# Kernel optimization log

Measured on AMD Instinct MI355X. Metric: run time of the kernel, lower is better.

The kernel has to match this reference:

```python
import jax, jax.numpy as jnp
import numpy as np

QUANT_DEPTH = 4
EMBED_DIM = 256
N_EMBED = 8192
B, H, W = 8, 32, 32


def setup_inputs() -> dict:
    key = jax.random.key(0)
    k1, k2 = jax.random.split(key)
    x = jax.random.normal(k1, (B, H, W, EMBED_DIM), dtype=jnp.float32)
    codebooks = jax.random.normal(k2, (QUANT_DEPTH, N_EMBED, EMBED_DIM), dtype=jnp.float32)
    return {"x": x, "codebooks": codebooks}


def _nearest_code(flat, cb):
    # flat: [N, D], cb: [K, D] -> idx: [N]
    # ||v - c||^2 = ||v||^2 + ||c||^2 - 2 v.c  (addmm in torch source)
    d = (jnp.sum(flat * flat, axis=1, keepdims=True)
         + jnp.sum(cb * cb, axis=1)[None, :]
         - 2.0 * (flat @ cb.T))  # [N, K]
    return jnp.argmin(d, axis=1)


def reference(x, codebooks):
    Bx, h, w, D = x.shape
    # quantization path is entirely non-differentiable (torch: detach + no_grad)
    resid = jax.lax.stop_gradient(x)
    agg = jnp.zeros_like(resid)
    quant_list = []
    code_list = []
    for i in range(codebooks.shape[0]):
        cb = codebooks[i]                      # [K, D]
        idx = _nearest_code(resid.reshape(-1, D), cb)  # [N]
        quant = cb[idx].reshape(Bx, h, w, D)
        resid = resid - quant
        agg = agg + quant
        quant_list.append(agg)
        code_list.append(idx.reshape(Bx, h, w, 1))
    codes = jnp.concatenate(code_list, axis=-1)  # [B, h, w, depth]
    # commitment loss: mean over depths of mean((x - agg_i.detach())^2)
    commitment_loss = jnp.mean(
        jnp.stack([jnp.mean((x - jax.lax.stop_gradient(q)) ** 2) for q in quant_list]))
    # straight-through estimator
    quants_trunc = x + jax.lax.stop_gradient(quant_list[-1] - x)
    return quants_trunc, commitment_loss, codes
```

## Files before the change

### kernel.cpp

```cpp
#include <hip/hip_runtime.h>

#define DIM   256
#define NVEC  8192
#define NCODE 8192
#define DEPTH 4

#define KBLK  8
#define KC    (NCODE / KBLK)
#define KT    (KC / 128)
#define FCAP  8192
#define FKS   32
#define FV    8
#define KAPPA 0.018f

typedef short  b8 __attribute__((ext_vector_type(8)));
typedef short  b4 __attribute__((ext_vector_type(4)));
typedef float  f4 __attribute__((ext_vector_type(4)));

static __device__ __forceinline__ unsigned short f2bf(float f) {
  unsigned u = __float_as_uint(f);
  return (unsigned short)((u + 0x7FFFu + ((u >> 16) & 1u)) >> 16);
}

static __device__ __forceinline__ void gll16(const void* g, void* l) {
  __builtin_amdgcn_global_load_lds(
      (const __attribute__((address_space(1))) void*)g,
      (__attribute__((address_space(3))) void*)l, 16, 0, 0);
}

__global__ __launch_bounds__(256) void prep_norms(const float* __restrict__ cb_all,
                                                  float* __restrict__ cc,
                                                  float* __restrict__ cchat) {
  int row  = blockIdx.x * 4 + (threadIdx.x >> 6);
  int lane = threadIdx.x & 63;
  float4 v = *(const float4*)&cb_all[(size_t)row * DIM + lane * 4];
  float st = 0.f, sh = 0.f;
  float vv[4] = {v.x, v.y, v.z, v.w};
  #pragma unroll
  for (int j = 0; j < 4; ++j) {
    float hf = __uint_as_float(((unsigned)f2bf(vv[j])) << 16);
    st += vv[j] * vv[j];
    sh += hf * hf;
  }
  #pragma unroll
  for (int off = 32; off > 0; off >>= 1) {
    st += __shfl_down(st, off, 64);
    sh += __shfl_down(sh, off, 64);
  }
  if (lane == 0) { cc[row] = st; cchat[row] = sh; }
}

__global__ __launch_bounds__(256) void prep_depth(const float* __restrict__ cbd,
                                                  unsigned short* __restrict__ cbh,
                                                  float* __restrict__ cbT) {
  __shared__ float ts[64][68];
  const int kb = blockIdx.x >> 2, db = blockIdx.x & 3;
  const int k0 = kb * 64, d0 = db * 64;
  const int t  = threadIdx.x;
  const int r  = t >> 2;
  const int c4 = (t & 3) * 16;

  const float* src = cbd + (size_t)(k0 + r) * DIM + d0 + c4;
  float4 q[4];
  #pragma unroll
  for (int i = 0; i < 4; ++i) q[i] = *(const float4*)(src + i * 4);

  b8 h0, h1;
  #pragma unroll
  for (int j = 0; j < 4; ++j) { h0[j] = (short)f2bf(q[0][j]); h0[4 + j] = (short)f2bf(q[1][j]); }
  #pragma unroll
  for (int j = 0; j < 4; ++j) { h1[j] = (short)f2bf(q[2][j]); h1[4 + j] = (short)f2bf(q[3][j]); }
  *(b8*)&cbh[(size_t)(k0 + r) * DIM + d0 + c4]     = h0;
  *(b8*)&cbh[(size_t)(k0 + r) * DIM + d0 + c4 + 8] = h1;

  #pragma unroll
  for (int i = 0; i < 4; ++i)
    #pragma unroll
    for (int j = 0; j < 4; ++j)
      ts[c4 + i * 4 + j][r] = q[i][j];
  __syncthreads();

  const int dd = t >> 2, kk4 = (t & 3) * 16;
  float* dst = cbT + (size_t)(d0 + dd) * NCODE + k0 + kk4;
  #pragma unroll
  for (int q4 = 0; q4 < 4; ++q4)
    *(float4*)(dst + q4 * 4) = *(const float4*)&ts[dd][kk4 + q4 * 4];
}

__global__ __launch_bounds__(256) void init_kernel(const float* __restrict__ x,
                                                   float* __restrict__ resid,
                                                   unsigned short* __restrict__ rb,
                                                   float* __restrict__ rsum0) {
  int n    = blockIdx.x * 4 + (threadIdx.x >> 6);
  int lane = threadIdx.x & 63;
  float4 v = *(const float4*)&x[(size_t)n * DIM + lane * 4];
  *(float4*)&resid[(size_t)n * DIM + lane * 4] = v;
  b4 hv; hv[0] = (short)f2bf(v.x); hv[1] = (short)f2bf(v.y);
  hv[2] = (short)f2bf(v.z); hv[3] = (short)f2bf(v.w);
  *(b4*)&rb[(size_t)n * DIM + lane * 4] = hv;
  float s = v.x * v.x + v.y * v.y + v.z * v.z + v.w * v.w;
  #pragma unroll
  for (int off = 32; off > 0; off >>= 1) s += __shfl_down(s, off, 64);
  if (lane == 0) rsum0[n] = s;
}

__global__ __launch_bounds__(512, 2) void coarse_kernel(
    const unsigned short* __restrict__ rb,
    const unsigned short* __restrict__ cbh,
    const float* __restrict__ cchat,
    float* __restrict__ pv1, int* __restrict__ pi1, float* __restrict__ pv2,
    int* __restrict__ fcount) {
  __shared__ __align__(16) char lds[65536];

  const int tid  = threadIdx.x;
  const int w    = tid >> 6;
  const int l    = tid & 63;
  const int mw   = w >> 1, kw = w & 1;
  const int mblk = blockIdx.x / KBLK;
  const int kblk = blockIdx.x % KBLK;
  const int m0   = mblk * 128;
  const int K0   = kblk * KC;

  if (blockIdx.x == 0 && tid == 0) *fcount = 0;

  int aoff[2], boff[2], ldst[2];
  #pragma unroll
  for (int it = 0; it < 2; ++it) {
    int o = it * 512 + tid;
    int row = o >> 3, ssl = (o & 7) ^ (row & 7);
    aoff[it] = (m0 + row) * 512 + ssl * 16;
    boff[it] = (K0 + row) * 512 + ssl * 16;
    ldst[it] = o * 16;
  }
  int offA[2][2], offB[4][2];
  #pragma unroll
  for (int mf = 0; mf < 2; ++mf) {
    int row = mw * 32 + mf * 16 + (l & 15);
    int base = row * 128 + (((l >> 4) ^ (row & 7)) * 16);
    offA[mf][0] = base; offA[mf][1] = base ^ 64;
  }
  #pragma unroll
  for (int nf = 0; nf < 4; ++nf) {
    int row = kw * 64 + nf * 16 + (l & 15);
    int base = row * 128 + (((l >> 4) ^ (row & 7)) * 16);
    offB[nf][0] = base; offB[nf][1] = base ^ 64;
  }

  const int kgb = K0 + kw * 64 + (l & 15);

  float tv1[8], tv2[8];
  int   ti1[8];
  #pragma unroll
  for (int s = 0; s < 8; ++s) { tv1[s] = 3.4e38f; tv2[s] = 3.4e38f; ti1[s] = 0; }

  f4 acc[2][4];
  b8 ar[4][2][2];

  #pragma unroll
  for (int it = 0; it < 2; ++it) {
    gll16((const char*)rb  + aoff[it], lds + ldst[it]);
    gll16((const char*)cbh + boff[it], lds + 16384 + ldst[it]);
  }
  __syncthreads();

  for (int kt = 0; kt < KT; ++kt) {
    #pragma unroll
    for (int dt = 0; dt < 4; ++dt) {
      const int buf = dt & 1;
      if (!(kt == KT - 1 && dt == 3)) {
        const int ndt = (dt + 1) & 3;
        const int nb  = ndt & 1;
        const int nktoff = (dt == 3) ? (kt + 1) * 65536 : kt * 65536;
        if (kt == 0 && dt < 3) {
          #pragma unroll
          for (int it = 0; it < 2; ++it)
            gll16((const char*)rb + aoff[it] + ndt * 128,
                  lds + nb * 32768 + ldst[it]);
        }
        #pragma unroll
        for (int it = 0; it < 2; ++it)
          gll16((const char*)cbh + boff[it] + nktoff + ndt * 128,
                lds + nb * 32768 + 16384 + ldst[it]);
      }
      if (dt == 0) {
        #pragma unroll
        for (int i = 0; i < 2; ++i)
          #pragma unroll
          for (int j = 0; j < 4; ++j)
            acc[i][j] = (f4){0.f, 0.f, 0.f, 0.f};
      }
      #pragma unroll
      for (int kk = 0; kk < 2; ++kk) {
        b8 af[2], bb[4];
        if (kt == 0) {
          #pragma unroll
          for (int mf = 0; mf < 2; ++mf) {
            af[mf] = *(const b8*)(lds + buf * 32768 + offA[mf][kk]);
            ar[dt][kk][mf] = af[mf];
          }
        } else {
          #pragma unroll
          for (int mf = 0; mf < 2; ++mf) af[mf] = ar[dt][kk][mf];
        }
        #pragma unroll
        for (int nf = 0; nf < 4; ++nf)
          bb[nf] = *(const b8*)(lds + buf * 32768 + 16384 + offB[nf][kk]);
        #pragma unroll
        for (int mf = 0; mf < 2; ++mf)
          #pragma unroll
          for (int nf = 0; nf < 4; ++nf)
            acc[mf][nf] = __builtin_amdgcn_mfma_f32_16x16x32_bf16(
                af[mf], bb[nf], acc[mf][nf], 0, 0, 0);
      }
      if (dt == 3) {
        float cn[4]; int kg[4];
        #pragma unroll
        for (int nf = 0; nf < 4; ++nf) {
          kg[nf] = kgb + kt * 128 + nf * 16;
          cn[nf] = cchat[kg[nf]];
        }
        #pragma unroll
        for (int mf = 0; mf < 2; ++mf)
          #pragma unroll
          for (int r = 0; r < 4; ++r) {
            const int s0 = mf * 4 + r;
            #pragma unroll
            for (int nf = 0; nf < 4; ++nf) {
              float s = fmaf(-2.f, acc[mf][nf][r], cn[nf]);
              bool  c = s < tv1[s0];
              float m2 = fminf(tv2[s0], s);
              tv2[s0] = c ? tv1[s0] : m2;
              ti1[s0] = c ? kg[nf] : ti1[s0];
              tv1[s0] = c ? s : tv1[s0];
            }
          }
      }
      __syncthreads();
    }
  }

  float* Mv1 = (float*)lds;
  int*   Mi1 = (int*)(lds + 1024);
  float* Mv2 = (float*)(lds + 2048);

  #pragma unroll
  for (int s0 = 0; s0 < 8; ++s0) {
    float v1 = tv1[s0], v2 = tv2[s0];
    int   i1 = ti1[s0];
    #pragma unroll
    for (int m = 1; m < 16; m <<= 1) {
      float qv1 = __shfl_xor(v1, m);
      int   qi1 = __shfl_xor(i1, m);
      float qv2 = __shfl_xor(v2, m);
      bool  qw  = (qv1 < v1) || (qv1 == v1 && qi1 < i1);
      float lose = qw ? v1 : qv1;
      float wv2  = qw ? qv2 : v2;
      v2 = fminf(wv2, lose);
      if (qw) { v1 = qv1; i1 = qi1; }
    }
    if ((l & 15) == 0) {
      int mf = s0 >> 2, r = s0 & 3;
      int rowL = mw * 32 + mf * 16 + (l >> 4) * 4 + r;
      Mv1[rowL * 2 + kw] = v1; Mi1[rowL * 2 + kw] = i1; Mv2[rowL * 2 + kw] = v2;
    }
  }
  __syncthreads();
  if (tid < 128) {
    float a1 = Mv1[tid * 2],     a2 = Mv2[tid * 2];     int a1i = Mi1[tid * 2];
    float b1 = Mv1[tid * 2 + 1], b2 = Mv2[tid * 2 + 1]; int b1i = Mi1[tid * 2 + 1];
    bool  bw = (b1 < a1) || (b1 == a1 && b1i < a1i);
    float v1 = bw ? b1 : a1; int i1 = bw ? b1i : a1i;
    float v2 = fminf(bw ? b2 : a2, bw ? a1 : b1);
    int n = m0 + tid;
    pv1[kblk * NVEC + n] = v1;
    pi1[kblk * NVEC + n] = i1;
    pv2[kblk * NVEC + n] = v2;
  }
}

__global__ __launch_bounds__(256) void merge_kernel(
    const float* __restrict__ pv1, const int* __restrict__ pi1,
    const float* __restrict__ pv2, const float* __restrict__ vnorm,
    int* __restrict__ idx, int* __restrict__ flist, int* __restrict__ fslot,
    int* __restrict__ fcount) {
  int n = blockIdx.x * 256 + threadIdx.x;
  float v1 = 3.4e38f, v2 = 3.4e38f; int i1 = 0;
  #pragma unroll
  for (int kb = 0; kb < KBLK; ++kb) {
    float b1 = pv1[kb * NVEC + n]; int b1i = pi1[kb * NVEC + n];
    float b2 = pv2[kb * NVEC + n];
    bool  bw = (b1 < v1) || (b1 == v1 && b1i < i1);
    float lose = bw ? v1 : b1;
    float wv2  = bw ? b2 : v2;
    v2 = fminf(wv2, lose);
    if (bw) { v1 = b1; i1 = b1i; }
  }
  idx[n] = i1;
  float thr = KAPPA * sqrtf(fmaxf(v1 + vnorm[n], 0.f)) + 1e-5f;
  int slot = -1;
  if (v2 - v1 < thr) {
    slot = atomicAdd(fcount, 1);
    flist[slot] = n;
  }
  fslot[n] = slot;
}

__global__ __launch_bounds__(256, 4) void fb_scan_t(
    const float* __restrict__ cbT, const float* __restrict__ cc,
    const float* __restrict__ resid, const int* __restrict__ flist,
    const int* __restrict__ fcount,
    float* __restrict__ fpv, int* __restrict__ fpi) {
  __shared__ float vsT[DIM][FV + 4];
  __shared__ float mv[FV][4];
  __shared__ int   mi[FV][4];
  const int cnt = min(*fcount, FCAP);
  const int ks = blockIdx.x & (FKS - 1);
  const int t = threadIdx.x;
  const int w = t >> 6, l = t & 63;
  const int k = ks * 256 + t;
  const float cn = cc[k];

  for (int chunk = blockIdx.x >> 5; chunk * FV < cnt; chunk += 256) {
    __syncthreads();
    #pragma unroll
    for (int v = 0; v < FV; ++v) {
      int s = chunk * FV + v;
      int n = flist[s < cnt ? s : chunk * FV];
      vsT[t][v] = resid[(size_t)n * DIM + t];
    }
    __syncthreads();

    float dot[FV];
    #pragma unroll
    for (int v = 0; v < FV; ++v) dot[v] = 0.f;

    #pragma unroll 8
    for (int d = 0; d < DIM; ++d) {
      float cv = cbT[(size_t)d * NCODE + k];
      f4 a0 = *(const f4*)&vsT[d][0];
      f4 a1 = *(const f4*)&vsT[d][4];
      dot[0] = fmaf(cv, a0[0], dot[0]);
      dot[1] = fmaf(cv, a0[1], dot[1]);
      dot[2] = fmaf(cv, a0[2], dot[2]);
      dot[3] = fmaf(cv, a0[3], dot[3]);
      dot[4] = fmaf(cv, a1[0], dot[4]);
      dot[5] = fmaf(cv, a1[1], dot[5]);
      dot[6] = fmaf(cv, a1[2], dot[6]);
      dot[7] = fmaf(cv, a1[3], dot[7]);
    }

    #pragma unroll
    for (int v = 0; v < FV; ++v) {
      float bv = fmaf(-2.f, dot[v], cn);
      int   bi = k;
      #pragma unroll
      for (int m = 1; m < 64; m <<= 1) {
        float qv = __shfl_xor(bv, m);
        int   qi = __shfl_xor(bi, m);
        if (qv < bv || (qv == bv && qi < bi)) { bv = qv; bi = qi; }
      }
      if (l == 0) { mv[v][w] = bv; mi[v][w] = bi; }
    }
    __syncthreads();
    if (t < FV) {
      float bv = mv[t][0]; int bi = mi[t][0];
      #pragma unroll
      for (int ww = 1; ww < 4; ++ww) {
        float qv = mv[t][ww]; int qi = mi[t][ww];
        if (qv < bv || (qv == bv && qi < bi)) { bv = qv; bi = qi; }
      }
      if (chunk * FV + t < cnt) {
        fpv[(size_t)(chunk * FV + t) * FKS + ks] = bv;
        fpi[(size_t)(chunk * FV + t) * FKS + ks] = bi;
      }
    }
  }
}

__global__ __launch_bounds__(256) void update_kernel(
    const float* __restrict__ cb, const int* __restrict__ idx,
    const int* __restrict__ fslot,
    const float* __restrict__ fpv, const int* __restrict__ fpi,
    float* __restrict__ resid, unsigned short* __restrict__ rb,
    float* __restrict__ rsum_out, float* __restrict__ codes_out, int depth) {
  int n    = blockIdx.x * 4 + (threadIdx.x >> 6);
  int lane = threadIdx.x & 63;
  int s    = fslot[n];
  int bi;
  if (s >= 0) {
    float v = 3.4e38f; int ii = 0x7fffffff;
    if (lane < FKS) { v = fpv[(size_t)s * FKS + lane]; ii = fpi[(size_t)s * FKS + lane]; }
    #pragma unroll
    for (int m = 1; m < FKS; m <<= 1) {
      float qv = __shfl_xor(v, m);
      int   qi = __shfl_xor(ii, m);
      if (qv < v || (qv == v && qi < ii)) { v = qv; ii = qi; }
    }
    bi = __shfl(ii, 0, 64);
  } else {
    bi = idx[n];
  }
  float4 q = *(const float4*)&cb[(size_t)bi * DIM + lane * 4];
  float4 r = *(float4*)&resid[(size_t)n * DIM + lane * 4];
  r.x -= q.x; r.y -= q.y; r.z -= q.z; r.w -= q.w;
  *(float4*)&resid[(size_t)n * DIM + lane * 4] = r;
  b4 hv; hv[0] = (short)f2bf(r.x); hv[1] = (short)f2bf(r.y);
  hv[2] = (short)f2bf(r.z); hv[3] = (short)f2bf(r.w);
  *(b4*)&rb[(size_t)n * DIM + lane * 4] = hv;
  float s2 = r.x * r.x + r.y * r.y + r.z * r.z + r.w * r.w;
  #pragma unroll
  for (int off = 32; off > 0; off >>= 1) s2 += __shfl_down(s2, off, 64);
  if (lane == 0) {
    rsum_out[n] = s2;
    codes_out[n * DEPTH + depth] = (float)bi;
  }
}

__global__ __launch_bounds__(256) void finalize(const float* __restrict__ x,
                                                float* __restrict__ out,
                                                const float* __restrict__ rsumL) {
  int i = blockIdx.x * blockDim.x + threadIdx.x;
  float4 r  = *(float4*)&out[(size_t)i * 4];
  float4 xv = *(const float4*)&x[(size_t)i * 4];
  float4 o;
  o.x = xv.x - r.x; o.y = xv.y - r.y; o.z = xv.z - r.z; o.w = xv.w - r.w;
  *(float4*)&out[(size_t)i * 4] = o;

  if (blockIdx.x == 0) {
    __shared__ float sm[256];
    float s = 0.f;
    for (int j = threadIdx.x; j < DEPTH * NVEC; j += 256) s += rsumL[j];
    sm[threadIdx.x] = s;
    __syncthreads();
    for (int off = 128; off > 0; off >>= 1) {
      if (threadIdx.x < off) sm[threadIdx.x] += sm[threadIdx.x + off];
      __syncthreads();
    }
    if (threadIdx.x == 0)
      out[NVEC * DIM] = sm[0] / (float)DEPTH / (float)(NVEC * DIM);
  }
}

extern "C" void kernel_launch(void* const* d_in, const int* in_sizes, int n_in,
                              void* d_out, int out_size, void* d_ws, size_t ws_size,
                              hipStream_t stream) {
  const float* x  = (const float*)d_in[0];
  const float* cb = (const float*)d_in[1];
  float* out = (float*)d_out;
  char*  wsb = (char*)d_ws;

  unsigned short* cbh = (unsigned short*)(wsb);
  unsigned short* rb  = (unsigned short*)(wsb + 4194304);
  float* cbT   = (float*)(wsb + 8388608);
  float* cc    = (float*)(wsb + 16777216);
  float* cchat = (float*)(wsb + 16908288);
  float* pv1   = (float*)(wsb + 17039360);
  int*   pi1   = (int*)  (wsb + 17563648);
  float* pv2   = (float*)(wsb + 18087936);
  float* rsum  = (float*)(wsb + 18612224);
  int*   idx   = (int*)  (wsb + 18776064);
  int*   flist = (int*)  (wsb + 18808832);
  int*   fslot = (int*)  (wsb + 18841600);
  int*   fcount= (int*)  (wsb + 18874368);
  float* fpv   = (float*)(wsb + 18878464);
  int*   fpi   = (int*)  (wsb + 19927040);

  float* resid     = out;
  float* codes_out = out + NVEC * DIM + 1;

  prep_norms<<<(DEPTH * NCODE) / 4, 256, 0, stream>>>(cb, cc, cchat);
  init_kernel<<<NVEC / 4, 256, 0, stream>>>(x, resid, rb, rsum);

  for (int d = 0; d < DEPTH; ++d) {
    const size_t cbo = (size_t)d * NCODE * DIM;
    prep_depth<<<512, 256, 0, stream>>>(cb + cbo, cbh, cbT);
    coarse_kernel<<<(NVEC / 128) * KBLK, 512, 0, stream>>>(
        rb, cbh, cchat + d * NCODE, pv1, pi1, pv2, fcount);
    merge_kernel<<<NVEC / 256, 256, 0, stream>>>(
        pv1, pi1, pv2, rsum + d * NVEC, idx, flist, fslot, fcount);
    fb_scan_t<<<256 * FKS, 256, 0, stream>>>(
        cbT, cc + d * NCODE, resid, flist, fcount, fpv, fpi);
    update_kernel<<<NVEC / 4, 256, 0, stream>>>(
        cb + cbo, idx, fslot, fpv, fpi, resid, rb,
        rsum + (d + 1) * NVEC, codes_out, d);
  }
  finalize<<<(NVEC * DIM / 4) / 256, 256, 0, stream>>>(x, out, rsum + NVEC);
}
```

Measured before the change: 467.8 us.

## Fuse merge into coarse kernel via last-block reduction, shrink fallback grid

The separate merge kernel is folded into coarse_kernel. Each of the KBLK blocks for a row tile bumps an atomic counter, and the last one to finish merges the per-kblock top-2 candidates and builds the fallback list. This removes one launch per depth. fcount is now reset in init/update, and the top-2 tracking in the inner loop uses fmed3/fmin instead of selects. The fallback scan grid is halved from 256 to 128 chunk-strides per k-slice, which cuts idle blocks but leaves each block more chunks to loop over when many vectors are flagged.

Result: slower. 872.7 us (+86.5%).

```diff
diff --git a/kernel.cpp b/kernel.cpp
--- a/kernel.cpp
+++ b/kernel.cpp
@@ -11,6 +11,7 @@
 #define FCAP  8192
 #define FKS   32
 #define FV    8
+#define FCH   128
 #define KAPPA 0.018f
 
 typedef short  b8 __attribute__((ext_vector_type(8)));
@@ -90,7 +91,9 @@
 __global__ __launch_bounds__(256) void init_kernel(const float* __restrict__ x,
                                                    float* __restrict__ resid,
                                                    unsigned short* __restrict__ rb,
-                                                   float* __restrict__ rsum0) {
+                                                   float* __restrict__ rsum0,
+                                                   int* __restrict__ zint) {
+  if (blockIdx.x == 0 && threadIdx.x < 128) zint[threadIdx.x] = 0;
   int n    = blockIdx.x * 4 + (threadIdx.x >> 6);
   int lane = threadIdx.x & 63;
   float4 v = *(const float4*)&x[(size_t)n * DIM + lane * 4];
@@ -109,8 +112,11 @@
     const unsigned short* __restrict__ cbh,
     const float* __restrict__ cchat,
     float* __restrict__ pv1, int* __restrict__ pi1, float* __restrict__ pv2,
-    int* __restrict__ fcount) {
+    const float* __restrict__ vnorm,
+    int* __restrict__ idx, int* __restrict__ flist, int* __restrict__ fslot,
+    int* __restrict__ fcount, int* __restrict__ done) {
   __shared__ __align__(16) char lds[65536];
+  __shared__ int lastBlk;
 
   const int tid  = threadIdx.x;
   const int w    = tid >> 6;
@@ -121,8 +127,6 @@
   const int m0   = mblk * 128;
   const int K0   = kblk * KC;
 
-  if (blockIdx.x == 0 && tid == 0) *fcount = 0;
-
   int aoff[2], boff[2], ldst[2];
   #pragma unroll
   for (int it = 0; it < 2; ++it) {
@@ -228,10 +232,9 @@
             for (int nf = 0; nf < 4; ++nf) {
               float s = fmaf(-2.f, acc[mf][nf][r], cn[nf]);
               bool  c = s < tv1[s0];
-              float m2 = fminf(tv2[s0], s);
-              tv2[s0] = c ? tv1[s0] : m2;
+              tv2[s0] = __builtin_amdgcn_fmed3f(s, tv1[s0], tv2[s0]);
               ti1[s0] = c ? kg[nf] : ti1[s0];
-              tv1[s0] = c ? s : tv1[s0];
+              tv1[s0] = fminf(tv1[s0], s);
             }
           }
       }
@@ -276,33 +279,38 @@
     pi1[kblk * NVEC + n] = i1;
     pv2[kblk * NVEC + n] = v2;
   }
-}
-
-__global__ __launch_bounds__(256) void merge_kernel(
-    const float* __restrict__ pv1, const int* __restrict__ pi1,
-    const float* __restrict__ pv2, const float* __restrict__ vnorm,
-    int* __restrict__ idx, int* __restrict__ flist, int* __restrict__ fslot,
-    int* __restrict__ fcount) {
-  int n = blockIdx.x * 256 + threadIdx.x;
-  float v1 = 3.4e38f, v2 = 3.4e38f; int i1 = 0;
-  #pragma unroll
-  for (int kb = 0; kb < KBLK; ++kb) {
-    float b1 = pv1[kb * NVEC + n]; int b1i = pi1[kb * NVEC + n];
-    float b2 = pv2[kb * NVEC + n];
-    bool  bw = (b1 < v1) || (b1 == v1 && b1i < i1);
-    float lose = bw ? v1 : b1;
-    float wv2  = bw ? b2 : v2;
-    v2 = fminf(wv2, lose);
-    if (bw) { v1 = b1; i1 = b1i; }
-  }
-  idx[n] = i1;
-  float thr = KAPPA * sqrtf(fmaxf(v1 + vnorm[n], 0.f)) + 1e-5f;
-  int slot = -1;
-  if (v2 - v1 < thr) {
-    slot = atomicAdd(fcount, 1);
-    flist[slot] = n;
-  }
-  fslot[n] = slot;
+
+  __threadfence();
+  __syncthreads();
+  if (tid == 0)
+    lastBlk = (atomicAdd(&done[mblk], 1) == KBLK - 1);
+  __syncthreads();
+  if (lastBlk) {
+    __threadfence();
+    if (tid == 0) done[mblk] = 0;
+    if (tid < 128) {
+      int n = m0 + tid;
+      float v1 = 3.4e38f, v2 = 3.4e38f; int i1 = 0;
+      #pragma unroll
+      for (int kb = 0; kb < KBLK; ++kb) {
+        float b1 = pv1[kb * NVEC + n]; int b1i = pi1[kb * NVEC + n];
+        float b2 = pv2[kb * NVEC + n];
+        bool  bw = (b1 < v1) || (b1 == v1 && b1i < i1);
+        float lose = bw ? v1 : b1;
+        float wv2  = bw ? b2 : v2;
+        v2 = fminf(wv2, lose);
+        if (bw) { v1 = b1; i1 = b1i; }
+      }
+      idx[n] = i1;
+      float thr = KAPPA * sqrtf(fmaxf(v1 + vnorm[n], 0.f)) + 1e-5f;
+      int slot = -1;
+      if (v2 - v1 < thr) {
+        slot = atomicAdd(fcount, 1);
+        flist[slot] = n;
+      }
+      fslot[n] = slot;
+    }
+  }
 }
 
 __global__ __launch_bounds__(256, 4) void fb_scan_t(
@@ -320,7 +328,7 @@
   const int k = ks * 256 + t;
   const float cn = cc[k];
 
-  for (int chunk = blockIdx.x >> 5; chunk * FV < cnt; chunk += 256) {
+  for (int chunk = blockIdx.x >> 5; chunk * FV < cnt; chunk += FCH) {
     __syncthreads();
     #pragma unroll
     for (int v = 0; v < FV; ++v) {
@@ -382,7 +390,9 @@
     const int* __restrict__ fslot,
     const float* __restrict__ fpv, const int* __restrict__ fpi,
     float* __restrict__ resid, unsigned short* __restrict__ rb,
-    float* __restrict__ rsum_out, float* __restrict__ codes_out, int depth) {
+    float* __restrict__ rsum_out, float* __restrict__ codes_out, int depth,
+    int* __restrict__ fcount) {
+  if (blockIdx.x == 0 && threadIdx.x == 0) *fcount = 0;
   int n    = blockIdx.x * 4 + (threadIdx.x >> 6);
   int lane = threadIdx.x & 63;
   int s    = fslot[n];
@@ -462,6 +472,7 @@
   int*   flist = (int*)  (wsb + 18808832);
   int*   fslot = (int*)  (wsb + 18841600);
   int*   fcount= (int*)  (wsb + 18874368);
+  int*   done  = (int*)  (wsb + 18874368 + 256);
   float* fpv   = (float*)(wsb + 18878464);
   int*   fpi   = (int*)  (wsb + 19927040);
 
@@ -469,20 +480,19 @@
   float* codes_out = out + NVEC * DIM + 1;
 
   prep_norms<<<(DEPTH * NCODE) / 4, 256, 0, stream>>>(cb, cc, cchat);
-  init_kernel<<<NVEC / 4, 256, 0, stream>>>(x, resid, rb, rsum);
+  init_kernel<<<NVEC / 4, 256, 0, stream>>>(x, resid, rb, rsum, fcount);
 
   for (int d = 0; d < DEPTH; ++d) {
     const size_t cbo = (size_t)d * NCODE * DIM;
     prep_depth<<<512, 256, 0, stream>>>(cb + cbo, cbh, cbT);
     coarse_kernel<<<(NVEC / 128) * KBLK, 512, 0, stream>>>(
-        rb, cbh, cchat + d * NCODE, pv1, pi1, pv2, fcount);
-    merge_kernel<<<NVEC / 256, 256, 0, stream>>>(
-        pv1, pi1, pv2, rsum + d * NVEC, idx, flist, fslot, fcount);
-    fb_scan_t<<<256 * FKS, 256, 0, stream>>>(
+        rb, cbh, cchat + d * NCODE, pv1, pi1, pv2,
+        rsum + d * NVEC, idx, flist, fslot, fcount, done);
+    fb_scan_t<<<FCH * FKS, 256, 0, stream>>>(
         cbT, cc + d * NCODE, resid, flist, fcount, fpv, fpi);
     update_kernel<<<NVEC / 4, 256, 0, stream>>>(
         cb + cbo, idx, fslot, fpv, fpi, resid, rb,
-        rsum + (d + 1) * NVEC, codes_out, d);
+        rsum + (d + 1) * NVEC, codes_out, d, fcount);
   }
   finalize<<<(NVEC * DIM / 4) / 256, 256, 0, stream>>>(x, out, rsum + NVEC);
 }
```
